# Optimization experiments

Hardware: AMD Instinct MI355X
Metric: run time of the kernel (lower is better)

Reference implementation:

```python
import jax, jax.numpy as jnp
import numpy as np

BS = 16384      # batch of tree nodes
N_CH = 8        # children per node (= max_output_degree)
H = 256         # h_size
RANK = 16       # tensor-train rank
N_AGGR = 4      # parallel aggregators
T = 64          # t_size (type embedding dim)
SCALE = 0.05    # param init scale (keeps the length-8 matmul chain stable)


def setup_inputs() -> dict:
    key = jax.random.key(0)
    ks = jax.random.split(key, 8)
    R = (RANK + 1) * RANK
    return {
        "neighbour_h": jax.random.normal(ks[0], (BS, N_CH, H), jnp.float32),
        "type_embs": jax.random.normal(ks[1], (BS, T), jnp.float32),
        "U": jax.random.normal(ks[2], (N_CH, N_AGGR, H, R), jnp.float32) * SCALE,
        "b": jax.random.normal(ks[3], (N_CH, N_AGGR, 1, R), jnp.float32) * SCALE,
        "U_type": jax.random.normal(ks[4], (N_AGGR, T, RANK), jnp.float32) * SCALE,
        "b_type": jax.random.normal(ks[5], (N_AGGR, 1, RANK), jnp.float32) * SCALE,
        "U_output": jax.random.normal(ks[6], (N_AGGR, RANK, H), jnp.float32) * SCALE,
        "b_output": jax.random.normal(ks[7], (N_AGGR, 1, H), jnp.float32) * SCALE,
    }


def reference(neighbour_h, type_embs, U, b, U_type, b_type, U_output, b_output):
    bs, n_ch, h = neighbour_h.shape
    n_aggr, _, rank = U_type.shape

    # per-child projection to TT cores: [bs, n_ch, n_aggr, (rank+1)*rank]
    ris = jnp.einsum('bch,cahr->bcar', neighbour_h, U[:n_ch]) + b[:n_ch, :, 0, :]
    ris = ris.reshape(bs, n_ch, n_aggr, rank + 1, rank)

    # initial rank vector from type embeddings: [bs, n_aggr, rank]
    rank_ris0 = jnp.einsum('bt,atr->bar', type_embs, U_type) + b_type[:, 0, :]

    # sequential TT chain over children (loop-carried dependency) via scan
    xs = jnp.moveaxis(ris, 1, 0)  # [n_ch, bs, n_aggr, rank+1, rank]

    def step(carry, aux):
        U_rank = aux[:, :, :-1, :]   # [bs, n_aggr, rank, rank]
        b_rank = aux[:, :, -2, :]    # row -2 (matches torch's aux[:,:,-2:-1,:])
        return jnp.einsum('bar,barq->baq', carry, U_rank) + b_rank, None

    rank_ris, _ = jax.lax.scan(step, rank_ris0, xs)

    # output projection: [bs, n_aggr, h]
    out = jnp.einsum('bar,arh->bah', rank_ris, U_output) + b_output[:, 0, :]
    return out.reshape(bs, n_aggr * h)
```

## Files before the change

kernel.cpp:

```cpp
#include <hip/hip_runtime.h>


#define N_CH   8
#define H_DIM  256
#define RANK_  16
#define N_AGGR 4
#define T_DIM  64
#define R_FULL 272
#define R_USE  256

typedef __bf16 bf16x8 __attribute__((ext_vector_type(8)));
typedef float  f32x4  __attribute__((ext_vector_type(4)));

union BF8 {
  bf16x8 v;
  unsigned short s[8];
  uint4 q;
};

static __device__ __forceinline__ unsigned short f2bf(float x) {
  union { float f; unsigned int u; } t; t.f = x;
  unsigned int u = t.u;
  return (unsigned short)((u + 0x7FFFu + ((u >> 16) & 1u)) >> 16);
}

__global__ void prep_U_kernel(const float* __restrict__ U, unsigned int* __restrict__ Ubf) {
  unsigned int idx = blockIdx.x * 256u + threadIdx.x;
  unsigned int r  = idx & 255u;
  unsigned int hp = (idx >> 8) & 127u;
  unsigned int ca = idx >> 15;
  const float* src = U + (size_t)(ca * 256u + 2u * hp) * 272u + r;
  unsigned int lo = f2bf(src[0]);
  unsigned int hi = f2bf(src[272]);
  Ubf[(ca * 256u + r) * 128u + hp] = lo | (hi << 16);
}

__global__ __launch_bounds__(256, 1)
void tt_main(const float* __restrict__ nh,
             const float* __restrict__ ty,
             const unsigned short* __restrict__ Ubf,
             const float* __restrict__ bB,
             const float* __restrict__ Ut,
             const float* __restrict__ bt,
             const float* __restrict__ Uo,
             const float* __restrict__ bo,
             float* __restrict__ out)
{
  const int lane = threadIdx.x & 63;
  const int a    = threadIdx.x >> 6;
  const int b0   = blockIdx.x * 64;
  const int lr   = lane & 15;
  const int lg   = lane >> 4;

  f32x4 carry[4];
  {
    float btv = bt[a * 16 + lr];
    BF8 utf[2];
#pragma unroll
    for (int ks = 0; ks < 2; ++ks)
#pragma unroll
      for (int j = 0; j < 8; ++j)
        utf[ks].s[j] = f2bf(Ut[a * 1024 + (ks * 32 + lg * 8 + j) * 16 + lr]);
#pragma unroll
    for (int mt = 0; mt < 4; ++mt) {
      f32x4 acc = { btv, btv, btv, btv };
#pragma unroll
      for (int ks = 0; ks < 2; ++ks) {
        BF8 af;
        const float* src = ty + (size_t)(b0 + mt * 16 + lr) * 64 + ks * 32 + lg * 8;
#pragma unroll
        for (int j = 0; j < 8; ++j) af.s[j] = f2bf(src[j]);
        acc = __builtin_amdgcn_mfma_f32_16x16x32_bf16(af.v, utf[ks].v, acc, 0, 0, 0);
      }
      carry[mt] = acc;
    }
  }

#pragma unroll 1
  for (int c = 0; c < N_CH; ++c) {
    BF8 Af[4][8];
#pragma unroll
    for (int mt = 0; mt < 4; ++mt)
#pragma unroll
      for (int ks = 0; ks < 8; ++ks) {
        const float* src = nh + (size_t)(b0 + mt * 16 + lr) * (N_CH * H_DIM)
                              + c * H_DIM + ks * 32 + lg * 8;
        float4 x0 = *(const float4*)(src);
        float4 x1 = *(const float4*)(src + 4);
        BF8 f;
        f.s[0] = f2bf(x0.x); f.s[1] = f2bf(x0.y); f.s[2] = f2bf(x0.z); f.s[3] = f2bf(x0.w);
        f.s[4] = f2bf(x1.x); f.s[5] = f2bf(x1.y); f.s[6] = f2bf(x1.z); f.s[7] = f2bf(x1.w);
        Af[mt][ks] = f;
      }

    const float* bBc = bB + (c * 4 + a) * R_FULL;
    const unsigned short* Ub = Ubf + (size_t)(c * 4 + a) * 65536;

    f32x4 partial[4];
#pragma unroll
    for (int mt = 0; mt < 4; ++mt) partial[mt] = { 0.f, 0.f, 0.f, 0.f };

    BF8 Bf0[8], Bf1[8];
#pragma unroll
    for (int ks = 0; ks < 8; ++ks)
      Bf0[ks].q = *(const uint4*)(Ub + (size_t)lr * 256 + ks * 32 + lg * 8);

#pragma unroll 1
    for (int tp = 0; tp < 8; ++tp) {
      const int t0 = 2 * tp, t1 = 2 * tp + 1;
#pragma unroll
      for (int ks = 0; ks < 8; ++ks)
        Bf1[ks].q = *(const uint4*)(Ub + (size_t)(t1 * 16 + lr) * 256 + ks * 32 + lg * 8);
      {
        float bias = bBc[t0 * 16 + lr];
        f32x4 acc[4];
#pragma unroll
        for (int mt = 0; mt < 4; ++mt) acc[mt] = { bias, bias, bias, bias };
#pragma unroll
        for (int ks = 0; ks < 8; ++ks)
#pragma unroll
          for (int mt = 0; mt < 4; ++mt)
            acc[mt] = __builtin_amdgcn_mfma_f32_16x16x32_bf16(Af[mt][ks].v, Bf0[ks].v, acc[mt], 0, 0, 0);
        const int srcl = (lane & 48) | t0;
#pragma unroll
        for (int mt = 0; mt < 4; ++mt)
#pragma unroll
          for (int i = 0; i < 4; ++i) {
            float cv = __shfl(carry[mt][i], srcl, 64);
            partial[mt][i] += cv * acc[mt][i];
          }
      }
      if (tp < 7) {
#pragma unroll
        for (int ks = 0; ks < 8; ++ks)
          Bf0[ks].q = *(const uint4*)(Ub + (size_t)((t0 + 2) * 16 + lr) * 256 + ks * 32 + lg * 8);
      }
      {
        float bias = bBc[t1 * 16 + lr];
        float extra = (tp == 7) ? 1.0f : 0.0f;
        f32x4 acc[4];
#pragma unroll
        for (int mt = 0; mt < 4; ++mt) acc[mt] = { bias, bias, bias, bias };
#pragma unroll
        for (int ks = 0; ks < 8; ++ks)
#pragma unroll
          for (int mt = 0; mt < 4; ++mt)
            acc[mt] = __builtin_amdgcn_mfma_f32_16x16x32_bf16(Af[mt][ks].v, Bf1[ks].v, acc[mt], 0, 0, 0);
        const int srcl = (lane & 48) | t1;
#pragma unroll
        for (int mt = 0; mt < 4; ++mt)
#pragma unroll
          for (int i = 0; i < 4; ++i) {
            float cv = __shfl(carry[mt][i], srcl, 64) + extra;
            partial[mt][i] += cv * acc[mt][i];
          }
      }
    }
#pragma unroll
    for (int mt = 0; mt < 4; ++mt) carry[mt] = partial[mt];
  }

  float uo[4][16], bov[4];
#pragma unroll
  for (int chk = 0; chk < 4; ++chk) {
    bov[chk] = bo[a * 256 + chk * 64 + lane];
#pragma unroll
    for (int r = 0; r < 16; ++r)
      uo[chk][r] = Uo[(size_t)a * 4096 + r * 256 + chk * 64 + lane];
  }
#pragma unroll
  for (int mt = 0; mt < 4; ++mt)
#pragma unroll
    for (int g = 0; g < 4; ++g)
#pragma unroll
      for (int i = 0; i < 4; ++i) {
        const int m = mt * 16 + g * 4 + i;
        float cv[16];
#pragma unroll
        for (int r = 0; r < 16; ++r) cv[r] = __shfl(carry[mt][i], (g << 4) | r, 64);
#pragma unroll
        for (int chk = 0; chk < 4; ++chk) {
          float v = bov[chk];
#pragma unroll
          for (int r = 0; r < 16; ++r) v += cv[r] * uo[chk][r];
          out[(size_t)(b0 + m) * 1024 + a * 256 + chk * 64 + lane] = v;
        }
      }
}

extern "C" void kernel_launch(void* const* d_in, const int* in_sizes, int n_in,
                              void* d_out, int out_size, void* d_ws, size_t ws_size,
                              hipStream_t stream) {
  const float* nh = (const float*)d_in[0];
  const float* ty = (const float*)d_in[1];
  const float* U  = (const float*)d_in[2];
  const float* bB = (const float*)d_in[3];
  const float* Ut = (const float*)d_in[4];
  const float* bt = (const float*)d_in[5];
  const float* Uo = (const float*)d_in[6];
  const float* bo = (const float*)d_in[7];
  float* out = (float*)d_out;

  unsigned int* Ubf32 = (unsigned int*)d_ws;

  prep_U_kernel<<<4096, 256, 0, stream>>>(U, Ubf32);
  tt_main<<<256, 256, 0, stream>>>(nh, ty, (const unsigned short*)d_ws,
                                   bB, Ut, bt, Uo, bo, out);
}
```

Baseline: 430.2 us.

## Split K across 16 waves per block with LDS-staged activations and atomic carry reduction

```diff
diff --git a/kernel.cpp b/kernel.cpp
--- a/kernel.cpp
+++ b/kernel.cpp
@@ -1,191 +1,245 @@
 #include <hip/hip_runtime.h>
 
 
-#define N_CH   8
-#define H_DIM  256
-#define RANK_  16
-#define N_AGGR 4
-#define T_DIM  64
-#define R_FULL 272
-#define R_USE  256
+#define N_CH 8
 
 typedef __bf16 bf16x8 __attribute__((ext_vector_type(8)));
 typedef float  f32x4  __attribute__((ext_vector_type(4)));
 
-union BF8 {
-  bf16x8 v;
-  unsigned short s[8];
-  uint4 q;
-};
+union BF8 { bf16x8 v; unsigned short s[8]; uint4 q; };
 
 static __device__ __forceinline__ unsigned short f2bf(float x) {
-  union { float f; unsigned int u; } t; t.f = x;
-  unsigned int u = t.u;
-  return (unsigned short)((u + 0x7FFFu + ((u >> 16) & 1u)) >> 16);
-}
-
-__global__ void prep_U_kernel(const float* __restrict__ U, unsigned int* __restrict__ Ubf) {
-  unsigned int idx = blockIdx.x * 256u + threadIdx.x;
-  unsigned int r  = idx & 255u;
-  unsigned int hp = (idx >> 8) & 127u;
-  unsigned int ca = idx >> 15;
-  const float* src = U + (size_t)(ca * 256u + 2u * hp) * 272u + r;
-  unsigned int lo = f2bf(src[0]);
-  unsigned int hi = f2bf(src[272]);
-  Ubf[(ca * 256u + r) * 128u + hp] = lo | (hi << 16);
-}
-
-__global__ __launch_bounds__(256, 1)
-void tt_main(const float* __restrict__ nh,
-             const float* __restrict__ ty,
-             const unsigned short* __restrict__ Ubf,
-             const float* __restrict__ bB,
-             const float* __restrict__ Ut,
-             const float* __restrict__ bt,
-             const float* __restrict__ Uo,
-             const float* __restrict__ bo,
-             float* __restrict__ out)
+  union { float f; unsigned u; } t; t.f = x;
+  return (unsigned short)((t.u + 0x7FFFu + ((t.u >> 16) & 1u)) >> 16);
+}
+static __device__ __forceinline__ unsigned pk2(float a, float b) {
+  return (unsigned)f2bf(a) | ((unsigned)f2bf(b) << 16);
+}
+
+__global__ __launch_bounds__(256) void prep_U(const float* __restrict__ U,
+                                              unsigned* __restrict__ Ubf) {
+  __shared__ float tile[32][257];
+  const int ca = blockIdx.x >> 3;
+  const int ks = blockIdx.x & 7;
+  const int tid = threadIdx.x;
+#pragma unroll 4
+  for (int i = 0; i < 32; ++i)
+    tile[i][tid] = U[((size_t)(ca * 256 + ks * 32 + i)) * 272 + tid];
+  __syncthreads();
+  const int lane = tid & 63, tq = tid >> 6;
+  const int rl = lane & 15, q = lane >> 4;
+#pragma unroll
+  for (int tt = 0; tt < 4; ++tt) {
+    const int t = tt * 4 + tq;
+    float v[8];
+#pragma unroll
+    for (int j = 0; j < 8; ++j) v[j] = tile[q * 8 + j][t * 16 + rl];
+    uint4 o;
+    o.x = pk2(v[0], v[1]); o.y = pk2(v[2], v[3]);
+    o.z = pk2(v[4], v[5]); o.w = pk2(v[6], v[7]);
+    *(uint4*)(Ubf + ((((size_t)ca * 16 + t) * 8 + ks) << 8) + lane * 4) = o;
+  }
+}
+
+#define LDS_A0 0
+#define LDS_A1 33792
+#define EXF 4352
+
+__global__ __launch_bounds__(1024) void tt_main(
+    const float* __restrict__ nh,
+    const float* __restrict__ ty,
+    const unsigned short* __restrict__ Ubf,
+    const float* __restrict__ bB,
+    const float* __restrict__ Ut,
+    const float* __restrict__ bt,
+    const float* __restrict__ Uo,
+    const float* __restrict__ bo,
+    float* __restrict__ out)
 {
-  const int lane = threadIdx.x & 63;
-  const int a    = threadIdx.x >> 6;
+  extern __shared__ char smem[];
+  __shared__ __align__(16) float EXs[3 * EXF];
+
+  const int tid  = threadIdx.x;
+  const int lane = tid & 63;
+  const int w    = tid >> 6;
+  const int a    = w & 3;
+  const int kq   = w >> 2;
   const int b0   = blockIdx.x * 64;
-  const int lr   = lane & 15;
-  const int lg   = lane >> 4;
-
-  f32x4 carry[4];
+  const int rl   = lane & 15;
+  const int q    = lane >> 4;
+
+  const float4 f0 = make_float4(0.f, 0.f, 0.f, 0.f);
+
+  for (int i = tid; i < 3264; i += 1024) ((float4*)EXs)[i] = f0;
+
   {
-    float btv = bt[a * 16 + lr];
+    const int row = tid >> 4, kb = (tid & 15) * 16;
+    const float* s = nh + ((size_t)(b0 + row) * N_CH + 0) * 256 + kb;
+    float4 x0 = ((const float4*)s)[0], x1 = ((const float4*)s)[1];
+    float4 x2 = ((const float4*)s)[2], x3 = ((const float4*)s)[3];
+    uint4 o0, o1;
+    o0.x = pk2(x0.x, x0.y); o0.y = pk2(x0.z, x0.w);
+    o0.z = pk2(x1.x, x1.y); o0.w = pk2(x1.z, x1.w);
+    o1.x = pk2(x2.x, x2.y); o1.y = pk2(x2.z, x2.w);
+    o1.z = pk2(x3.x, x3.y); o1.w = pk2(x3.z, x3.w);
+    *(uint4*)(smem + LDS_A0 + row * 528 + kb * 2)      = o0;
+    *(uint4*)(smem + LDS_A0 + row * 528 + kb * 2 + 16) = o1;
+  }
+  __syncthreads();
+
+  if (kq == 0) {
     BF8 utf[2];
 #pragma unroll
-    for (int ks = 0; ks < 2; ++ks)
+    for (int ks2 = 0; ks2 < 2; ++ks2)
 #pragma unroll
       for (int j = 0; j < 8; ++j)
-        utf[ks].s[j] = f2bf(Ut[a * 1024 + (ks * 32 + lg * 8 + j) * 16 + lr]);
-#pragma unroll
-    for (int mt = 0; mt < 4; ++mt) {
-      f32x4 acc = { btv, btv, btv, btv };
-#pragma unroll
-      for (int ks = 0; ks < 2; ++ks) {
-        BF8 af;
-        const float* src = ty + (size_t)(b0 + mt * 16 + lr) * 64 + ks * 32 + lg * 8;
-#pragma unroll
-        for (int j = 0; j < 8; ++j) af.s[j] = f2bf(src[j]);
-        acc = __builtin_amdgcn_mfma_f32_16x16x32_bf16(af.v, utf[ks].v, acc, 0, 0, 0);
+        utf[ks2].s[j] = f2bf(Ut[a * 1024 + (ks2 * 32 + q * 8 + j) * 16 + rl]);
+    const float4 bt4 = *(const float4*)(bt + a * 16 + q * 4);
+#pragma unroll
+    for (int nt = 0; nt < 4; ++nt) {
+      f32x4 acc = { bt4.x, bt4.y, bt4.z, bt4.w };
+#pragma unroll
+      for (int ks2 = 0; ks2 < 2; ++ks2) {
+        const float* s = ty + (size_t)(b0 + nt * 16 + rl) * 64 + ks2 * 32 + q * 8;
+        float4 y0 = ((const float4*)s)[0], y1 = ((const float4*)s)[1];
+        BF8 bf;
+        bf.s[0] = f2bf(y0.x); bf.s[1] = f2bf(y0.y); bf.s[2] = f2bf(y0.z); bf.s[3] = f2bf(y0.w);
+        bf.s[4] = f2bf(y1.x); bf.s[5] = f2bf(y1.y); bf.s[6] = f2bf(y1.z); bf.s[7] = f2bf(y1.w);
+        acc = __builtin_amdgcn_mfma_f32_16x16x32_bf16(utf[ks2].v, bf.v, acc, 0, 0, 0);
       }
-      carry[mt] = acc;
-    }
-  }
+#pragma unroll
+      for (int i = 0; i < 4; ++i)
+        atomicAdd(&EXs[a * 1088 + (q * 4 + i) * 68 + nt * 16 + rl], acc[i]);
+    }
+  }
+  __syncthreads();
+
+  float4 sg0, sg1, sg2, sg3;
 
 #pragma unroll 1
   for (int c = 0; c < N_CH; ++c) {
-    BF8 Af[4][8];
-#pragma unroll
-    for (int mt = 0; mt < 4; ++mt)
-#pragma unroll
-      for (int ks = 0; ks < 8; ++ks) {
-        const float* src = nh + (size_t)(b0 + mt * 16 + lr) * (N_CH * H_DIM)
-                              + c * H_DIM + ks * 32 + lg * 8;
-        float4 x0 = *(const float4*)(src);
-        float4 x1 = *(const float4*)(src + 4);
-        BF8 f;
-        f.s[0] = f2bf(x0.x); f.s[1] = f2bf(x0.y); f.s[2] = f2bf(x0.z); f.s[3] = f2bf(x0.w);
-        f.s[4] = f2bf(x1.x); f.s[5] = f2bf(x1.y); f.s[6] = f2bf(x1.z); f.s[7] = f2bf(x1.w);
-        Af[mt][ks] = f;
-      }
-
-    const float* bBc = bB + (c * 4 + a) * R_FULL;
-    const unsigned short* Ub = Ubf + (size_t)(c * 4 + a) * 65536;
+    const int cur = c % 3, nxt = (c + 1) % 3, zro = (c + 2) % 3;
+    const float* exC = EXs + cur * EXF + a * 1088;
+    float*       exN = EXs + nxt * EXF + a * 1088;
+    const int aCur = (c & 1) ? LDS_A1 : LDS_A0;
+    const int aNxt = (c & 1) ? LDS_A0 : LDS_A1;
+
+    BF8 Nf[4][2];
+#pragma unroll
+    for (int nt = 0; nt < 4; ++nt)
+#pragma unroll
+      for (int s2 = 0; s2 < 2; ++s2)
+        Nf[nt][s2].q = *(const uint4*)(smem + aCur + (nt * 16 + rl) * 528 +
+                                       (2 * kq + s2) * 64 + q * 16);
+
+    for (int i = tid; i < 1088; i += 1024) ((float4*)(EXs + zro * EXF))[i] = f0;
+
+    const unsigned short* Uc = Ubf + (size_t)(c * 4 + a) * 65536;
+    const float* bBp = bB + (c * 4 + a) * 272;
+    uint4 Ur[2][2]; float4 bb[2];
+#pragma unroll
+    for (int h2 = 0; h2 < 2; ++h2) {
+      const unsigned short* up = Uc + h2 * 4096 + 2 * kq * 512 + lane * 8;
+      Ur[h2][0] = *(const uint4*)up;
+      Ur[h2][1] = *(const uint4*)(up + 512);
+      bb[h2] = (kq == 0) ? *(const float4*)(bBp + h2 * 16 + q * 4) : f0;
+    }
 
     f32x4 partial[4];
 #pragma unroll
-    for (int mt = 0; mt < 4; ++mt) partial[mt] = { 0.f, 0.f, 0.f, 0.f };
-
-    BF8 Bf0[8], Bf1[8];
-#pragma unroll
-    for (int ks = 0; ks < 8; ++ks)
-      Bf0[ks].q = *(const uint4*)(Ub + (size_t)lr * 256 + ks * 32 + lg * 8);
+    for (int nt = 0; nt < 4; ++nt) partial[nt] = { 0.f, 0.f, 0.f, 0.f };
 
 #pragma unroll 1
     for (int tp = 0; tp < 8; ++tp) {
-      const int t0 = 2 * tp, t1 = 2 * tp + 1;
-#pragma unroll
-      for (int ks = 0; ks < 8; ++ks)
-        Bf1[ks].q = *(const uint4*)(Ub + (size_t)(t1 * 16 + lr) * 256 + ks * 32 + lg * 8);
-      {
-        float bias = bBc[t0 * 16 + lr];
+#pragma unroll
+      for (int half = 0; half < 2; ++half) {
+        const int t = tp * 2 + half;
+        const float* cvp = exC + t * 68 + rl;
+        float cv0 = cvp[0], cv1 = cvp[16], cv2 = cvp[32], cv3 = cvp[48];
+        BF8 ua0, ua1; ua0.q = Ur[half][0]; ua1.q = Ur[half][1];
+        const float4 bs = bb[half];
         f32x4 acc[4];
 #pragma unroll
-        for (int mt = 0; mt < 4; ++mt) acc[mt] = { bias, bias, bias, bias };
-#pragma unroll
-        for (int ks = 0; ks < 8; ++ks)
-#pragma unroll
-          for (int mt = 0; mt < 4; ++mt)
-            acc[mt] = __builtin_amdgcn_mfma_f32_16x16x32_bf16(Af[mt][ks].v, Bf0[ks].v, acc[mt], 0, 0, 0);
-        const int srcl = (lane & 48) | t0;
-#pragma unroll
-        for (int mt = 0; mt < 4; ++mt)
-#pragma unroll
-          for (int i = 0; i < 4; ++i) {
-            float cv = __shfl(carry[mt][i], srcl, 64);
-            partial[mt][i] += cv * acc[mt][i];
-          }
+        for (int nt = 0; nt < 4; ++nt) acc[nt] = { bs.x, bs.y, bs.z, bs.w };
+#pragma unroll
+        for (int nt = 0; nt < 4; ++nt)
+          acc[nt] = __builtin_amdgcn_mfma_f32_16x16x32_bf16(ua0.v, Nf[nt][0].v, acc[nt], 0, 0, 0);
+#pragma unroll
+        for (int nt = 0; nt < 4; ++nt)
+          acc[nt] = __builtin_amdgcn_mfma_f32_16x16x32_bf16(ua1.v, Nf[nt][1].v, acc[nt], 0, 0, 0);
+        if (t < 14) {
+          const unsigned short* up = Uc + (size_t)(t + 2) * 4096 + 2 * kq * 512 + lane * 8;
+          Ur[half][0] = *(const uint4*)up;
+          Ur[half][1] = *(const uint4*)(up + 512);
+          if (kq == 0) bb[half] = *(const float4*)(bBp + (t + 2) * 16 + q * 4);
+        }
+        if (t == 14 && c < 7) {
+          const int row = tid >> 4, kb = (tid & 15) * 16;
+          const float* s = nh + ((size_t)(b0 + row) * N_CH + (c + 1)) * 256 + kb;
+          sg0 = ((const float4*)s)[0]; sg1 = ((const float4*)s)[1];
+          sg2 = ((const float4*)s)[2]; sg3 = ((const float4*)s)[3];
+        }
+        const float extra = (t == 15) ? 1.0f : 0.0f;
+        const float cva[4] = { cv0 + extra, cv1 + extra, cv2 + extra, cv3 + extra };
+#pragma unroll
+        for (int nt = 0; nt < 4; ++nt)
+#pragma unroll
+          for (int i = 0; i < 4; ++i)
+            partial[nt][i] += cva[nt] * acc[nt][i];
       }
-      if (tp < 7) {
-#pragma unroll
-        for (int ks = 0; ks < 8; ++ks)
-          Bf0[ks].q = *(const uint4*)(Ub + (size_t)((t0 + 2) * 16 + lr) * 256 + ks * 32 + lg * 8);
-      }
-      {
-        float bias = bBc[t1 * 16 + lr];
-        float extra = (tp == 7) ? 1.0f : 0.0f;
-        f32x4 acc[4];
-#pragma unroll
-        for (int mt = 0; mt < 4; ++mt) acc[mt] = { bias, bias, bias, bias };
-#pragma unroll
-        for (int ks = 0; ks < 8; ++ks)
-#pragma unroll
-          for (int mt = 0; mt < 4; ++mt)
-            acc[mt] = __builtin_amdgcn_mfma_f32_16x16x32_bf16(Af[mt][ks].v, Bf1[ks].v, acc[mt], 0, 0, 0);
-        const int srcl = (lane & 48) | t1;
-#pragma unroll
-        for (int mt = 0; mt < 4; ++mt)
-#pragma unroll
-          for (int i = 0; i < 4; ++i) {
-            float cv = __shfl(carry[mt][i], srcl, 64) + extra;
-            partial[mt][i] += cv * acc[mt][i];
-          }
-      }
-    }
-#pragma unroll
-    for (int mt = 0; mt < 4; ++mt) carry[mt] = partial[mt];
-  }
-
-  float uo[4][16], bov[4];
-#pragma unroll
-  for (int chk = 0; chk < 4; ++chk) {
-    bov[chk] = bo[a * 256 + chk * 64 + lane];
-#pragma unroll
-    for (int r = 0; r < 16; ++r)
-      uo[chk][r] = Uo[(size_t)a * 4096 + r * 256 + chk * 64 + lane];
-  }
-#pragma unroll
-  for (int mt = 0; mt < 4; ++mt)
-#pragma unroll
-    for (int g = 0; g < 4; ++g)
-#pragma unroll
-      for (int i = 0; i < 4; ++i) {
-        const int m = mt * 16 + g * 4 + i;
-        float cv[16];
-#pragma unroll
-        for (int r = 0; r < 16; ++r) cv[r] = __shfl(carry[mt][i], (g << 4) | r, 64);
-#pragma unroll
-        for (int chk = 0; chk < 4; ++chk) {
-          float v = bov[chk];
-#pragma unroll
-          for (int r = 0; r < 16; ++r) v += cv[r] * uo[chk][r];
-          out[(size_t)(b0 + m) * 1024 + a * 256 + chk * 64 + lane] = v;
-        }
-      }
+    }
+
+    if (c < 7) {
+      const int row = tid >> 4, kb = (tid & 15) * 16;
+      uint4 o0, o1;
+      o0.x = pk2(sg0.x, sg0.y); o0.y = pk2(sg0.z, sg0.w);
+      o0.z = pk2(sg1.x, sg1.y); o0.w = pk2(sg1.z, sg1.w);
+      o1.x = pk2(sg2.x, sg2.y); o1.y = pk2(sg2.z, sg2.w);
+      o1.z = pk2(sg3.x, sg3.y); o1.w = pk2(sg3.z, sg3.w);
+      *(uint4*)(smem + aNxt + row * 528 + kb * 2)      = o0;
+      *(uint4*)(smem + aNxt + row * 528 + kb * 2 + 16) = o1;
+    }
+
+#pragma unroll
+    for (int nt = 0; nt < 4; ++nt)
+#pragma unroll
+      for (int i = 0; i < 4; ++i)
+        atomicAdd(&exN[(q * 4 + i) * 68 + nt * 16 + rl], partial[nt][i]);
+    __syncthreads();
+  }
+
+  const float* exF = EXs + 2 * EXF + a * 1088;
+  BF8 Ae[4];
+#pragma unroll
+  for (int mt = 0; mt < 4; ++mt) {
+    uint4 zq; zq.x = zq.y = zq.z = zq.w = 0u;
+    Ae[mt].q = zq;
+    if (q < 2) {
+#pragma unroll
+      for (int j = 0; j < 8; ++j)
+        Ae[mt].s[j] = f2bf(exF[(q * 8 + j) * 68 + mt * 16 + rl]);
+    }
+  }
+#pragma unroll
+  for (int nt = 0; nt < 4; ++nt) {
+    const int hc = (4 * kq + nt) * 16;
+    BF8 Be;
+#pragma unroll
+    for (int j = 0; j < 8; ++j) {
+      float x = 0.f;
+      if (q < 2) x = Uo[a * 4096 + (q * 8 + j) * 256 + hc + rl];
+      Be.s[j] = (q < 2) ? f2bf(x) : (unsigned short)0;
+    }
+    const float bv = bo[a * 256 + hc + rl];
+#pragma unroll
+    for (int mt = 0; mt < 4; ++mt) {
+      f32x4 oacc = { bv, bv, bv, bv };
+      oacc = __builtin_amdgcn_mfma_f32_16x16x32_bf16(Ae[mt].v, Be.v, oacc, 0, 0, 0);
+#pragma unroll
+      for (int i = 0; i < 4; ++i)
+        out[(size_t)(b0 + mt * 16 + q * 4 + i) * 1024 + a * 256 + hc + rl] = oacc[i];
+    }
+  }
 }
 
 extern "C" void kernel_launch(void* const* d_in, const int* in_sizes, int n_in,
@@ -201,9 +255,12 @@
   const float* bo = (const float*)d_in[7];
   float* out = (float*)d_out;
 
-  unsigned int* Ubf32 = (unsigned int*)d_ws;
-
-  prep_U_kernel<<<4096, 256, 0, stream>>>(U, Ubf32);
-  tt_main<<<256, 256, 0, stream>>>(nh, ty, (const unsigned short*)d_ws,
-                                   bB, Ut, bt, Uo, bo, out);
-}
+  unsigned* Ubf32 = (unsigned*)d_ws;
+
+  prep_U<<<256, 256, 0, stream>>>(U, Ubf32);
+
+  (void)hipFuncSetAttribute((const void*)tt_main,
+                            hipFuncAttributeMaxDynamicSharedMemorySize, 67584);
+  tt_main<<<256, 1024, 67584, stream>>>(nh, ty, (const unsigned short*)d_ws,
+                                        bB, Ut, bt, Uo, bo, out);
+}
```

New measurement: 812.7 us. 88.9% more time.
